# Performance work log

Hardware: AMD Instinct MI355X
Metric: run time of the kernel (lower is better)

Reference implementation:

```python
import jax, jax.numpy as jnp
import numpy as np

N_NODES = 50000


def _pointnet_layer(h, pos, src, dst, wA, bA, wB, bB):
    # message: MLP(concat(h_j, pos_j - pos_i)) per edge, then max-aggregate at dst
    m = jnp.concatenate([h[src], pos[src] - pos[dst]], axis=-1)  # [E, in+3]
    m = jax.nn.relu(m @ wA + bA) @ wB + bB                       # [E, out]
    agg = jax.ops.segment_max(m, dst, num_segments=N_NODES)     # [N, out]
    # PyG max-aggregation returns 0 for nodes with no incoming edges
    return jnp.where(jnp.isfinite(agg), agg, 0.0)


def setup_inputs() -> dict:
    key = jax.random.key(0)
    ks = jax.random.split(key, 16)
    num_points, num_features, E = 256, 256, 800000
    s = 0.05
    inp = {
        "x": jax.random.normal(ks[0], (N_NODES, num_points), dtype=jnp.float32),
        "pos": jax.random.normal(ks[1], (N_NODES, 3), dtype=jnp.float32),
        "edge_index": jax.random.randint(ks[2], (2, E), 0, N_NODES, dtype=jnp.int64),
        # conv1 mlp: (num_points+3 -> F -> F)
        "w1a": jax.random.normal(ks[3], (num_points + 3, num_features), dtype=jnp.float32) * s,
        "b1a": jnp.zeros((num_features,), dtype=jnp.float32),
        "w1b": jax.random.normal(ks[4], (num_features, num_features), dtype=jnp.float32) * s,
        "b1b": jnp.zeros((num_features,), dtype=jnp.float32),
        # conv2 mlp: (F+3 -> F -> F)
        "w2a": jax.random.normal(ks[5], (num_features + 3, num_features), dtype=jnp.float32) * s,
        "b2a": jnp.zeros((num_features,), dtype=jnp.float32),
        "w2b": jax.random.normal(ks[6], (num_features, num_features), dtype=jnp.float32) * s,
        "b2b": jnp.zeros((num_features,), dtype=jnp.float32),
        # decoder: F -> 256 -> num_points
        "wd1": jax.random.normal(ks[7], (num_features, 256), dtype=jnp.float32) * s,
        "bd1": jnp.zeros((256,), dtype=jnp.float32),
        "wd2": jax.random.normal(ks[8], (256, num_points), dtype=jnp.float32) * s,
        "bd2": jnp.zeros((num_points,), dtype=jnp.float32),
    }
    return inp


def reference(x, pos, edge_index, w1a, b1a, w1b, b1b, w2a, b2a, w2b, b2b, wd1, bd1, wd2, bd2):
    src, dst = edge_index[0], edge_index[1]  # message flows j(src) -> i(dst)
    h = jax.nn.relu(_pointnet_layer(x, pos, src, dst, w1a, b1a, w1b, b1b))
    h = jax.nn.relu(_pointnet_layer(h, pos, src, dst, w2a, b2a, w2b, b2b))
    decoded = jax.nn.relu(h @ wd1 + bd1) @ wd2 + bd2  # [N, num_points]
    return decoded
```

## Files before the change

kernel.cpp:

```cpp
#include <hip/hip_runtime.h>
#include <stdint.h>


using bf16x8 = __attribute__((ext_vector_type(8))) short;
using f32x4  = __attribute__((ext_vector_type(4))) float;

#define AB_STRIDE 40
#define ABUF      2560
#define ZSTRIDE   68

#define BARRIER_NOVM() asm volatile("s_waitcnt lgkmcnt(0)\n\ts_barrier" ::: "memory")

__device__ __forceinline__ float b2f(uint32_t v16) {
    return __uint_as_float(v16 << 16);
}
__device__ __forceinline__ float b2f_hi(uint32_t w) {
    return __uint_as_float(w & 0xffff0000u);
}
__device__ __forceinline__ uint16_t f2b(float f) {
    uint32_t u = __float_as_uint(f);
    u += 0x7fffu + ((u >> 16) & 1u);
    return (uint16_t)(u >> 16);
}
#if __has_builtin(__builtin_amdgcn_cvt_pk_bf16_f32)
__device__ __forceinline__ uint32_t pack2bf(float lo, float hi) {
    auto r = __builtin_amdgcn_cvt_pk_bf16_f32(lo, hi);
    uint32_t u; __builtin_memcpy(&u, &r, 4); return u;
}
#else
__device__ __forceinline__ uint32_t pack2bf(float lo, float hi) {
    return (uint32_t)f2b(lo) | ((uint32_t)f2b(hi) << 16);
}
#endif
__device__ __forceinline__ uint32_t encf(float f) {
    uint32_t u = __float_as_uint(f);
    return (u & 0x80000000u) ? ~u : (u | 0x80000000u);
}
__device__ __forceinline__ float decf(uint32_t k) {
    uint32_t u = (k & 0x80000000u) ? (k & 0x7fffffffu) : ~k;
    return __uint_as_float(u);
}

__global__ void detect_fmt(const uint32_t* __restrict__ x,
                           const uint32_t* __restrict__ ei,
                           uint32_t* __restrict__ flags) {
    if (threadIdx.x == 0 && blockIdx.x == 0) {
        int plaus = 0;
        for (int i = 0; i < 64; i++) {
            uint32_t v = x[i];
            uint32_t e = (v >> 23) & 0xffu;
            if (v == 0u || (e >= 96u && e <= 150u)) plaus++;
        }
        flags[0] = (plaus >= 48) ? 1u : 0u;
        int zeros = 0;
        for (int i = 0; i < 16; i++)
            if (ei[2 * i + 1] == 0u) zeros++;
        flags[1] = (zeros == 16) ? 1u : 0u;
    }
}

__global__ __launch_bounds__(256) void convert_big(
        const void* __restrict__ src, uint16_t* __restrict__ dst, int n,
        const uint32_t* __restrict__ flags) {
    bool isf32 = flags[0] != 0u;
    int i = (blockIdx.x * 256 + threadIdx.x) * 4;
    if (i + 3 < n) {
        if (isf32) {
            float4 v = ((const float4*)src)[i >> 2];
            uint2 o = {pack2bf(v.x, v.y), pack2bf(v.z, v.w)};
            ((uint2*)dst)[i >> 2] = o;
        } else {
            ((uint2*)dst)[i >> 2] = ((const uint2*)src)[i >> 2];
        }
    } else {
        for (int j = i; j < n; j++)
            dst[j] = isf32 ? f2b(((const float*)src)[j]) : ((const uint16_t*)src)[j];
    }
}

struct ConvArgs {
    const void* src[13];
    uint32_t dstOff[13];
    uint32_t n[13];
};

__global__ __launch_bounds__(256) void convert_small(
        ConvArgs a, uint16_t* __restrict__ dstBase, const uint32_t* __restrict__ flags) {
    bool isf32 = flags[0] != 0u;
    int t = blockIdx.y;
    int i = blockIdx.x * 256 + threadIdx.x;
    if (i >= (int)a.n[t]) return;
    uint16_t* d = dstBase + a.dstOff[t];
    d[i] = isf32 ? f2b(((const float*)a.src[t])[i]) : ((const uint16_t*)a.src[t])[i];
}

__global__ __launch_bounds__(256) void zero_i32(int* p, int n) {
    int i = blockIdx.x * 256 + threadIdx.x;
    if (i < n) p[i] = 0;
}

__global__ __launch_bounds__(256) void hist_dst(
        const int* __restrict__ ei_raw, int E, int* __restrict__ hist,
        const uint32_t* __restrict__ flags) {
    bool i64 = flags[1] != 0u;
    int e = blockIdx.x * 256 + threadIdx.x;
    if (e < E) {
        int d = i64 ? ei_raw[2 * (E + e)] : ei_raw[E + e];
        atomicAdd(&hist[d], 1);
    }
}

__global__ __launch_bounds__(1024) void scan_partial(
        const int* __restrict__ hist, int* __restrict__ cursor,
        int* __restrict__ part, int N) {
    __shared__ int wsum[16];
    int tid = threadIdx.x, lane = tid & 63, wid = tid >> 6;
    int base = blockIdx.x * 1024;
    int v = (base + tid < N) ? hist[base + tid] : 0;
    int x = v;
#pragma unroll
    for (int s = 1; s < 64; s <<= 1) {
        int t = __shfl_up(x, s, 64);
        if (lane >= s) x += t;
    }
    if (lane == 63) wsum[wid] = x;
    __syncthreads();
    if (wid == 0 && lane < 16) {
        int w = wsum[lane];
#pragma unroll
        for (int s = 1; s < 16; s <<= 1) {
            int t = __shfl_up(w, s, 64);
            if (lane >= s) w += t;
        }
        wsum[lane] = w;
    }
    __syncthreads();
    int wbase = (wid > 0) ? wsum[wid - 1] : 0;
    if (base + tid < N) cursor[base + tid] = x - v + wbase;
    if (tid == 0) part[blockIdx.x] = wsum[15];
}

__global__ __launch_bounds__(1024) void scan_carry(
        const int* __restrict__ part, int* __restrict__ carry, int B) {
    __shared__ int wsum[16];
    int tid = threadIdx.x, lane = tid & 63, wid = tid >> 6;
    int v = (tid < B) ? part[tid] : 0;
    int x = v;
#pragma unroll
    for (int s = 1; s < 64; s <<= 1) {
        int t = __shfl_up(x, s, 64);
        if (lane >= s) x += t;
    }
    if (lane == 63) wsum[wid] = x;
    __syncthreads();
    if (wid == 0 && lane < 16) {
        int w = wsum[lane];
#pragma unroll
        for (int s = 1; s < 16; s <<= 1) {
            int t = __shfl_up(w, s, 64);
            if (lane >= s) w += t;
        }
        wsum[lane] = w;
    }
    __syncthreads();
    int wbase = (wid > 0) ? wsum[wid - 1] : 0;
    if (tid < B) carry[tid] = x - v + wbase;
}

__global__ __launch_bounds__(1024) void scan_add(
        int* __restrict__ cursor, const int* __restrict__ carry, int N) {
    int i = blockIdx.x * 1024 + threadIdx.x;
    if (i < N) cursor[i] += carry[blockIdx.x];
}

__global__ __launch_bounds__(256) void scatter_edges(
        const int* __restrict__ ei_raw, int E, int* __restrict__ cursor,
        int* __restrict__ esrc, int* __restrict__ edst,
        const uint32_t* __restrict__ flags) {
    bool i64 = flags[1] != 0u;
    int e = blockIdx.x * 256 + threadIdx.x;
    if (e < E) {
        int s = i64 ? ei_raw[2 * e] : ei_raw[e];
        int d = i64 ? ei_raw[2 * (E + e)] : ei_raw[E + e];
        int p = atomicAdd(&cursor[d], 1);
        esrc[p] = s;
        edst[p] = d;
    }
}

__global__ __launch_bounds__(256) void transpose_w(
        const uint16_t* s0, const uint16_t* s1, const uint16_t* s2,
        const uint16_t* s3, const uint16_t* s4, const uint16_t* s5,
        uint16_t* dst) {
    const uint16_t* srcs[6] = {s0, s1, s2, s3, s4, s5};
    const uint16_t* src = srcs[blockIdx.y];
    uint16_t* d = dst + (size_t)blockIdx.y * 65536;
    int k = blockIdx.x;
    int n = threadIdx.x;
    d[(k >> 5) * 8192 + n * 32 + (k & 31)] = src[k * 256 + n];
}

__global__ __launch_bounds__(256) void pos_proj(
        const uint16_t* pos, const uint16_t* wpos, uint16_t* Q, int N) {
    int t = threadIdx.x;
    int r = t >> 5, c8 = (t & 31) * 8;
    int i = blockIdx.x * 8 + r;
    if (i >= N) return;
    uint4 wv0 = *(const uint4*)(wpos + c8);
    uint4 wv1 = *(const uint4*)(wpos + 256 + c8);
    uint4 wv2 = *(const uint4*)(wpos + 512 + c8);
    float p0 = b2f(pos[i * 3 + 0]);
    float p1 = b2f(pos[i * 3 + 1]);
    float p2 = b2f(pos[i * 3 + 2]);
    uint32_t w0[4] = {wv0.x, wv0.y, wv0.z, wv0.w};
    uint32_t w1[4] = {wv1.x, wv1.y, wv1.z, wv1.w};
    uint32_t w2[4] = {wv2.x, wv2.y, wv2.z, wv2.w};
    uint32_t o[4];
#pragma unroll
    for (int j = 0; j < 4; j++) {
        float lo = p0 * b2f(w0[j] & 0xffffu) + p1 * b2f(w1[j] & 0xffffu) + p2 * b2f(w2[j] & 0xffffu);
        float hi = p0 * b2f_hi(w0[j]) + p1 * b2f_hi(w1[j]) + p2 * b2f_hi(w2[j]);
        o[j] = pack2bf(lo, hi);
    }
    uint4 ov = {o[0], o[1], o[2], o[3]};
    *(uint4*)(Q + (size_t)i * 256 + c8) = ov;
}

__global__ __launch_bounds__(256) void init_agg(uint32_t* agg, int n4) {
    int i = blockIdx.x * 256 + threadIdx.x;
    if (i < n4) {
        uint4 v = {0x80000000u, 0x80000000u, 0x80000000u, 0x80000000u};
        ((uint4*)agg)[i] = v;
    }
}

template <int REINIT>
__global__ __launch_bounds__(256) void finalize_init(
        uint32_t* __restrict__ agg, uint16_t* __restrict__ h, int n4) {
    int i = blockIdx.x * 256 + threadIdx.x;
    if (i < n4) {
        uint4 a = ((uint4*)agg)[i];
        uint2 o = {pack2bf(decf(a.x), decf(a.y)), pack2bf(decf(a.z), decf(a.w))};
        ((uint2*)h)[i] = o;
        if (REINIT) {
            uint4 z = {0x80000000u, 0x80000000u, 0x80000000u, 0x80000000u};
            ((uint4*)agg)[i] = z;
        }
    }
}

template <int MODE>
__global__ __launch_bounds__(256) void gemm_node(
        const uint16_t* __restrict__ A, const uint16_t* __restrict__ BT,
        const uint16_t* __restrict__ bias, const uint16_t* __restrict__ Qadd,
        void* __restrict__ out, int M, const uint32_t* __restrict__ flags) {
    __shared__ __align__(16) uint16_t Al[2 * 64 * AB_STRIDE];
    int tid = threadIdx.x;
    int tileM = blockIdx.x;
    int wave = tid >> 6, lane = tid & 63, lrow = lane & 15, quad = lane >> 4;
    int row = tid >> 2, kq = (tid & 3) * 8;
    f32x4 acc[4][4] = {};

    int rg = tileM * 64 + row;
    bool rok = rg < M;
    const uint16_t* abase = A + (size_t)rg * 256 + kq;
    const uint16_t* bfrag = BT + (wave * 64 + lrow) * 32 + quad * 8;
    uint16_t* awr = Al + row * AB_STRIDE + kq;
    const uint16_t* ard = Al + lrow * AB_STRIDE + quad * 8;

    uint4 a0 = {0, 0, 0, 0};
    if (rok) a0 = *(const uint4*)abase;

#pragma unroll
    for (int kc = 0; kc < 256; kc += 32) {
        int buf = (kc >> 5) & 1;
        *(uint4*)(awr + buf * ABUF) = a0;
        const uint16_t* bp = bfrag + (kc >> 5) * 8192;
        bf16x8 bfv[4];
#pragma unroll
        for (int c = 0; c < 4; c++) bfv[c] = *(const bf16x8*)(bp + c * 512);
        if (kc < 224 && rok) a0 = *(const uint4*)(abase + kc + 32);
        BARRIER_NOVM();
        const uint16_t* ar = ard + buf * ABUF;
        bf16x8 af[4];
#pragma unroll
        for (int r = 0; r < 4; r++) af[r] = *(const bf16x8*)(ar + r * 16 * AB_STRIDE);
#pragma unroll
        for (int r = 0; r < 4; r++)
#pragma unroll
            for (int c = 0; c < 4; c++)
                acc[r][c] = __builtin_amdgcn_mfma_f32_16x16x32_bf16(af[r], bfv[c], acc[r][c], 0, 0, 0);
    }

    bool of32 = false;
    if (MODE == 2) of32 = flags[0] != 0u;

#pragma unroll
    for (int c = 0; c < 4; c++) {
        int col = wave * 64 + c * 16 + lrow;
        float bv = b2f(bias[col]);
#pragma unroll
        for (int r = 0; r < 4; r++) {
#pragma unroll
            for (int i = 0; i < 4; i++) {
                int rw = tileM * 64 + r * 16 + quad * 4 + i;
                if (rw >= M) continue;
                float v = acc[r][c][i] + bv;
                if (MODE == 0) {
                    v += b2f(Qadd[(size_t)rw * 256 + col]);
                    ((uint16_t*)out)[(size_t)rw * 256 + col] = f2b(v);
                } else if (MODE == 1) {
                    v = fmaxf(v, 0.f);
                    ((uint16_t*)out)[(size_t)rw * 256 + col] = f2b(v);
                } else {
                    if (of32) ((float*)out)[(size_t)rw * 256 + col] = v;
                    else      ((uint16_t*)out)[(size_t)rw * 256 + col] = f2b(v);
                }
            }
        }
    }
}

__global__ __launch_bounds__(256, 3) void edge_gemm_agg(
        const uint16_t* __restrict__ Gs16, const uint16_t* __restrict__ Qb,
        const uint16_t* __restrict__ BT, const uint16_t* __restrict__ bias,
        const int* __restrict__ esrc, const int* __restrict__ edst, int E,
        uint32_t* __restrict__ agg) {
    __shared__ __align__(16) uint16_t SM[256 * ZSTRIDE];
    uint16_t* Al = SM;
    uint16_t* Zl = SM;
    __shared__ int sdst[64];
    __shared__ uint64_t smask;
    int tid = threadIdx.x;
    int ebase = blockIdx.x * 64;
    int evalid = (E - ebase < 64) ? (E - ebase) : 64;
    if (tid < 64) sdst[tid] = (tid < evalid) ? edst[ebase + tid] : 0;

    int wave = tid >> 6, lane = tid & 63, lrow = lane & 15, quad = lane >> 4;
    int row = tid >> 2, kq = (tid & 3) * 8;
    int er = (row < evalid) ? row : (evalid - 1);
    int s = esrc[ebase + er];
    int d = edst[ebase + er];
    const uint16_t* gbase = Gs16 + (size_t)s * 256 + kq;
    const uint16_t* qbase = Qb   + (size_t)d * 256 + kq;
    const uint16_t* bfrag = BT + (wave * 64 + lrow) * 32 + quad * 8;
    uint16_t* awr = Al + row * AB_STRIDE + kq;
    const uint16_t* ard = Al + lrow * AB_STRIDE + quad * 8;

    f32x4 acc[4][4] = {};
    uint4 g = *(const uint4*)gbase;
    uint4 q = *(const uint4*)qbase;

#pragma unroll
    for (int kc = 0; kc < 256; kc += 32) {
        int buf = (kc >> 5) & 1;
        uint32_t gw[4] = {g.x, g.y, g.z, g.w};
        uint32_t qw[4] = {q.x, q.y, q.z, q.w};
        uint32_t mw[4];
#pragma unroll
        for (int j = 0; j < 4; j++) {
            float lo = fmaxf(b2f(gw[j] & 0xffffu) - b2f(qw[j] & 0xffffu), 0.f);
            float hi = fmaxf(b2f_hi(gw[j]) - b2f_hi(qw[j]), 0.f);
            mw[j] = pack2bf(lo, hi);
        }
        uint4 wv = {mw[0], mw[1], mw[2], mw[3]};
        *(uint4*)(awr + buf * ABUF) = wv;
        const uint16_t* bp = bfrag + (kc >> 5) * 8192;
        bf16x8 bfv[4];
#pragma unroll
        for (int c = 0; c < 4; c++) bfv[c] = *(const bf16x8*)(bp + c * 512);
        if (kc < 224) {
            g = *(const uint4*)(gbase + kc + 32);
            q = *(const uint4*)(qbase + kc + 32);
        }
        BARRIER_NOVM();
        const uint16_t* ar = ard + buf * ABUF;
        bf16x8 af[4];
#pragma unroll
        for (int r = 0; r < 4; r++) af[r] = *(const bf16x8*)(ar + r * 16 * AB_STRIDE);
#pragma unroll
        for (int r = 0; r < 4; r++)
#pragma unroll
            for (int c = 0; c < 4; c++)
                acc[r][c] = __builtin_amdgcn_mfma_f32_16x16x32_bf16(af[r], bfv[c], acc[r][c], 0, 0, 0);
    }
    __syncthreads();

    float bv[4];
#pragma unroll
    for (int c = 0; c < 4; c++) bv[c] = b2f(bias[wave * 64 + c * 16 + lrow]);
#pragma unroll
    for (int c = 0; c < 4; c++) {
        int col = wave * 64 + c * 16 + lrow;
#pragma unroll
        for (int r = 0; r < 4; r++) {
            uint2 z4 = {pack2bf(acc[r][c][0] + bv[c], acc[r][c][1] + bv[c]),
                        pack2bf(acc[r][c][2] + bv[c], acc[r][c][3] + bv[c])};
            *(uint2*)&Zl[col * ZSTRIDE + r * 16 + quad * 4] = z4;
        }
    }
    if (wave == 0) {
        int d0 = sdst[lane];
        int dp = (lane > 0) ? sdst[lane - 1] : -1;
        uint64_t m = __ballot(d0 != dp);
        if (lane == 0) smask = m;
    }
    __syncthreads();

    uint64_t mask = smask;
    int col = tid;
    const uint16_t* zc = &Zl[col * ZSTRIDE];
    float run = 0.f;
#pragma unroll 4
    for (int gi = 0; gi < 16; gi++) {
        int rbase = gi * 4;
        if (rbase >= evalid) break;
        uint2 z4 = *(const uint2*)&zc[rbase];
        float vv[4] = {b2f(z4.x & 0xffffu), b2f_hi(z4.x),
                       b2f(z4.y & 0xffffu), b2f_hi(z4.y)};
#pragma unroll
        for (int i = 0; i < 4; i++) {
            int r = rbase + i;
            if (r >= evalid) break;
            if (r == 0) {
                run = vv[0];
            } else if ((mask >> r) & 1ull) {
                int dp = sdst[r - 1];
                atomicMax(agg + (size_t)dp * 256 + col, encf(run));
                run = vv[i];
            } else {
                run = fmaxf(run, vv[i]);
            }
        }
    }
    if (evalid > 0)
        atomicMax(agg + (size_t)sdst[evalid - 1] * 256 + col, encf(run));
}

extern "C" void kernel_launch(void* const* d_in, const int* in_sizes, int n_in,
                              void* d_out, int out_size, void* d_ws, size_t ws_size,
                              hipStream_t stream) {
    const void* x_raw   = d_in[0];
    const void* pos_raw = d_in[1];
    const int*  ei_raw  = (const int*)d_in[2];

    int N = in_sizes[0] / 256;
    int E = in_sizes[2] / 2;

    char* ws = (char*)d_ws;
    size_t off = 0;
    auto alloc = [&](size_t bytes) { void* p = ws + off; off += (bytes + 255) & ~(size_t)255; return p; };

    uint32_t* flags = (uint32_t*)alloc(256);
    uint16_t* WT    = (uint16_t*)alloc(6 * 65536 * sizeof(uint16_t));
    const uint32_t POS_OFF = 0;
    const uint32_t W1A_OFF = POS_OFF + (uint32_t)(N * 3);
    const uint32_t W2A_OFF = W1A_OFF + 66304;
    const uint32_t W1B_OFF = W2A_OFF + 66304;
    const uint32_t W2B_OFF = W1B_OFF + 65536;
    const uint32_t WD1_OFF = W2B_OFF + 65536;
    const uint32_t WD2_OFF = WD1_OFF + 65536;
    const uint32_t B1A_OFF = WD2_OFF + 65536;
    const uint32_t B1B_OFF = B1A_OFF + 256;
    const uint32_t B2A_OFF = B1B_OFF + 256;
    const uint32_t B2B_OFF = B2A_OFF + 256;
    const uint32_t BD1_OFF = B2B_OFF + 256;
    const uint32_t BD2_OFF = BD1_OFF + 256;
    const uint32_t ARENA_ELEMS = BD2_OFF + 256;
    uint16_t* arena = (uint16_t*)alloc((size_t)ARENA_ELEMS * 2);
    int*      hist  = (int*)alloc((size_t)N * 4);
    int*      curs  = (int*)alloc((size_t)N * 4);
    int*      part  = (int*)alloc(1024 * 4);
    int*      carry = (int*)alloc(1024 * 4);
    int*      esrc  = (int*)alloc((size_t)E * 4);
    int*      edst  = (int*)alloc((size_t)E * 4);
    uint16_t* Qb    = (uint16_t*)alloc((size_t)N * 256 * 2);
    uint16_t* Gs    = (uint16_t*)alloc((size_t)N * 256 * 2);
    uint32_t* agg   = (uint32_t*)alloc((size_t)N * 256 * 4);
    uint16_t* xb    = (uint16_t*)alloc((size_t)N * 256 * 2);
    uint16_t* h     = xb;
    uint16_t* d1    = Gs;

    uint16_t* posb = arena + POS_OFF;
    uint16_t* w1a = arena + W1A_OFF, * w2a = arena + W2A_OFF;
    uint16_t* w1b = arena + W1B_OFF, * w2b = arena + W2B_OFF;
    uint16_t* wd1 = arena + WD1_OFF, * wd2 = arena + WD2_OFF;
    uint16_t* b1a = arena + B1A_OFF, * b1b = arena + B1B_OFF;
    uint16_t* b2a = arena + B2A_OFF, * b2b = arena + B2B_OFF;
    uint16_t* bd1 = arena + BD1_OFF, * bd2 = arena + BD2_OFF;

    int n4      = N * 64;
    int nbElem  = (n4 + 255) / 256;
    int nbNode  = (N + 63) / 64;
    int nbEdge  = (E + 63) / 64;
    int nbE256  = (E + 255) / 256;
    int nbPos   = (N + 7) / 8;
    int nbScan  = (N + 1023) / 1024;

    detect_fmt<<<1, 64, 0, stream>>>((const uint32_t*)x_raw, (const uint32_t*)ei_raw, flags);
    convert_big<<<(N * 256 / 4 + 255) / 256, 256, 0, stream>>>(x_raw, xb, N * 256, flags);

    ConvArgs ca;
    ca.src[0] = pos_raw;  ca.dstOff[0] = POS_OFF; ca.n[0] = (uint32_t)(N * 3);
    ca.src[1] = d_in[3];  ca.dstOff[1] = W1A_OFF; ca.n[1] = 66304;
    ca.src[2] = d_in[7];  ca.dstOff[2] = W2A_OFF; ca.n[2] = 66304;
    ca.src[3] = d_in[5];  ca.dstOff[3] = W1B_OFF; ca.n[3] = 65536;
    ca.src[4] = d_in[9];  ca.dstOff[4] = W2B_OFF; ca.n[4] = 65536;
    ca.src[5] = d_in[11]; ca.dstOff[5] = WD1_OFF; ca.n[5] = 65536;
    ca.src[6] = d_in[13]; ca.dstOff[6] = WD2_OFF; ca.n[6] = 65536;
    ca.src[7] = d_in[4];  ca.dstOff[7] = B1A_OFF; ca.n[7] = 256;
    ca.src[8] = d_in[6];  ca.dstOff[8] = B1B_OFF; ca.n[8] = 256;
    ca.src[9] = d_in[8];  ca.dstOff[9] = B2A_OFF; ca.n[9] = 256;
    ca.src[10] = d_in[10]; ca.dstOff[10] = B2B_OFF; ca.n[10] = 256;
    ca.src[11] = d_in[12]; ca.dstOff[11] = BD1_OFF; ca.n[11] = 256;
    ca.src[12] = d_in[14]; ca.dstOff[12] = BD2_OFF; ca.n[12] = 256;
    {
        uint32_t maxn = (uint32_t)(N * 3);
        dim3 g((maxn + 255) / 256, 13);
        convert_small<<<g, 256, 0, stream>>>(ca, arena, flags);
    }

    zero_i32<<<(N + 255) / 256, 256, 0, stream>>>(hist, N);
    hist_dst<<<nbE256, 256, 0, stream>>>(ei_raw, E, hist, flags);
    scan_partial<<<nbScan, 1024, 0, stream>>>(hist, curs, part, N);
    scan_carry<<<1, 1024, 0, stream>>>(part, carry, nbScan);
    scan_add<<<nbScan, 1024, 0, stream>>>(curs, carry, N);
    scatter_edges<<<nbE256, 256, 0, stream>>>(ei_raw, E, curs, esrc, edst, flags);

    transpose_w<<<dim3(256, 6), 256, 0, stream>>>(w1a, w1b, w2a, w2b, wd1, wd2, WT);

    pos_proj<<<nbPos, 256, 0, stream>>>(posb, w1a + 65536, Qb, N);
    gemm_node<0><<<nbNode, 256, 0, stream>>>(xb, WT + 0 * 65536, b1a, Qb, Gs, N, flags);
    init_agg<<<nbElem, 256, 0, stream>>>(agg, n4);
    edge_gemm_agg<<<nbEdge, 256, 0, stream>>>(Gs, Qb, WT + 1 * 65536, b1b, esrc, edst, E, agg);
    finalize_init<1><<<nbElem, 256, 0, stream>>>(agg, h, n4);

    pos_proj<<<nbPos, 256, 0, stream>>>(posb, w2a + 65536, Qb, N);
    gemm_node<0><<<nbNode, 256, 0, stream>>>(h, WT + 2 * 65536, b2a, Qb, Gs, N, flags);
    edge_gemm_agg<<<nbEdge, 256, 0, stream>>>(Gs, Qb, WT + 3 * 65536, b2b, esrc, edst, E, agg);
    finalize_init<0><<<nbElem, 256, 0, stream>>>(agg, h, n4);

    gemm_node<1><<<nbNode, 256, 0, stream>>>(h, WT + 4 * 65536, bd1, nullptr, d1, N, flags);
    gemm_node<2><<<nbNode, 256, 0, stream>>>(d1, WT + 5 * 65536, bd2, nullptr, d_out, N, flags);
}
```

Baseline: 766.4 us.

## Fuse input conversion, aggregation finalize and re-init into node GEMM prologues

Drops the standalone kernel that converts x to bf16 and the finalize/init_agg kernels. The node GEMMs now read raw f32 x or the encoded max-aggregation buffer directly and convert while staging tiles into LDS. The first aggregation buffer is reset to the sentinel inside the second layer's GEMM, and hist zeroing is merged with agg init. This removes several full passes over N×256 arrays and the intermediate bf16 h buffer. In exchange the GEMMs read 32-bit A data (twice the bytes), carry extra conversion ALU work, and get a launch_bounds occupancy hint; the in-place agg reset depends on each block rereading only its own rows.

```diff
diff --git a/kernel.cpp b/kernel.cpp
--- a/kernel.cpp
+++ b/kernel.cpp
@@ -59,25 +59,6 @@
     }
 }
 
-__global__ __launch_bounds__(256) void convert_big(
-        const void* __restrict__ src, uint16_t* __restrict__ dst, int n,
-        const uint32_t* __restrict__ flags) {
-    bool isf32 = flags[0] != 0u;
-    int i = (blockIdx.x * 256 + threadIdx.x) * 4;
-    if (i + 3 < n) {
-        if (isf32) {
-            float4 v = ((const float4*)src)[i >> 2];
-            uint2 o = {pack2bf(v.x, v.y), pack2bf(v.z, v.w)};
-            ((uint2*)dst)[i >> 2] = o;
-        } else {
-            ((uint2*)dst)[i >> 2] = ((const uint2*)src)[i >> 2];
-        }
-    } else {
-        for (int j = i; j < n; j++)
-            dst[j] = isf32 ? f2b(((const float*)src)[j]) : ((const uint16_t*)src)[j];
-    }
-}
-
 struct ConvArgs {
     const void* src[13];
     uint32_t dstOff[13];
@@ -94,9 +75,20 @@
     d[i] = isf32 ? f2b(((const float*)a.src[t])[i]) : ((const uint16_t*)a.src[t])[i];
 }
 
-__global__ __launch_bounds__(256) void zero_i32(int* p, int n) {
+__global__ __launch_bounds__(256) void init_hist_agg(
+        uint32_t* __restrict__ agg, int n4, int* __restrict__ hist, int N) {
     int i = blockIdx.x * 256 + threadIdx.x;
-    if (i < n) p[i] = 0;
+    if (i < n4) {
+        uint4 v = {0x80000000u, 0x80000000u, 0x80000000u, 0x80000000u};
+        ((uint4*)agg)[i] = v;
+    }
+    int i4 = i * 4;
+    if (i4 + 3 < N) {
+        uint4 z = {0, 0, 0, 0};
+        ((uint4*)hist)[i] = z;
+    } else if (i4 < N) {
+        for (int j = i4; j < N; j++) hist[j] = 0;
+    }
 }
 
 __global__ __launch_bounds__(256) void hist_dst(
@@ -226,34 +218,12 @@
     *(uint4*)(Q + (size_t)i * 256 + c8) = ov;
 }
 
-__global__ __launch_bounds__(256) void init_agg(uint32_t* agg, int n4) {
-    int i = blockIdx.x * 256 + threadIdx.x;
-    if (i < n4) {
-        uint4 v = {0x80000000u, 0x80000000u, 0x80000000u, 0x80000000u};
-        ((uint4*)agg)[i] = v;
-    }
-}
-
-template <int REINIT>
-__global__ __launch_bounds__(256) void finalize_init(
-        uint32_t* __restrict__ agg, uint16_t* __restrict__ h, int n4) {
-    int i = blockIdx.x * 256 + threadIdx.x;
-    if (i < n4) {
-        uint4 a = ((uint4*)agg)[i];
-        uint2 o = {pack2bf(decf(a.x), decf(a.y)), pack2bf(decf(a.z), decf(a.w))};
-        ((uint2*)h)[i] = o;
-        if (REINIT) {
-            uint4 z = {0x80000000u, 0x80000000u, 0x80000000u, 0x80000000u};
-            ((uint4*)agg)[i] = z;
-        }
-    }
-}
-
-template <int MODE>
-__global__ __launch_bounds__(256) void gemm_node(
-        const uint16_t* __restrict__ A, const uint16_t* __restrict__ BT,
+template <int AMODE, int OUTMODE, int REINIT>
+__global__ __launch_bounds__(256, 3) void gemm_node(
+        const void* __restrict__ Araw, const uint16_t* __restrict__ BT,
         const uint16_t* __restrict__ bias, const uint16_t* __restrict__ Qadd,
-        void* __restrict__ out, int M, const uint32_t* __restrict__ flags) {
+        void* __restrict__ out, int M, const uint32_t* __restrict__ flags,
+        uint32_t* __restrict__ aggwb) {
     __shared__ __align__(16) uint16_t Al[2 * 64 * AB_STRIDE];
     int tid = threadIdx.x;
     int tileM = blockIdx.x;
@@ -263,23 +233,61 @@
 
     int rg = tileM * 64 + row;
     bool rok = rg < M;
-    const uint16_t* abase = A + (size_t)rg * 256 + kq;
+    int rgc = rok ? rg : (M - 1);
+    bool isf32 = false;
+    if (AMODE == 2 || OUTMODE == 2) isf32 = flags[0] != 0u;
+
+    const uint16_t* a16 = (const uint16_t*)Araw + (size_t)rgc * 256 + kq;
+    const uint32_t* a32 = (const uint32_t*)Araw + (size_t)rgc * 256 + kq;
     const uint16_t* bfrag = BT + (wave * 64 + lrow) * 32 + quad * 8;
     uint16_t* awr = Al + row * AB_STRIDE + kq;
     const uint16_t* ard = Al + lrow * AB_STRIDE + quad * 8;
 
-    uint4 a0 = {0, 0, 0, 0};
-    if (rok) a0 = *(const uint4*)abase;
+    uint4 p0 = {0, 0, 0, 0}, p1 = {0, 0, 0, 0};
+    if (AMODE == 0) {
+        p0 = *(const uint4*)a16;
+    } else if (AMODE == 1) {
+        p0 = *(const uint4*)a32; p1 = *(const uint4*)(a32 + 4);
+    } else {
+        if (isf32) { p0 = *(const uint4*)a32; p1 = *(const uint4*)(a32 + 4); }
+        else       { p0 = *(const uint4*)a16; }
+    }
 
 #pragma unroll
     for (int kc = 0; kc < 256; kc += 32) {
         int buf = (kc >> 5) & 1;
-        *(uint4*)(awr + buf * ABUF) = a0;
+        uint4 wv;
+        if (AMODE == 0 || (AMODE == 2 && !isf32)) {
+            wv = p0;
+        } else if (AMODE == 1) {
+            uint32_t a[8] = {p0.x, p0.y, p0.z, p0.w, p1.x, p1.y, p1.z, p1.w};
+            wv.x = pack2bf(decf(a[0]), decf(a[1]));
+            wv.y = pack2bf(decf(a[2]), decf(a[3]));
+            wv.z = pack2bf(decf(a[4]), decf(a[5]));
+            wv.w = pack2bf(decf(a[6]), decf(a[7]));
+        } else {
+            wv.x = pack2bf(__uint_as_float(p0.x), __uint_as_float(p0.y));
+            wv.y = pack2bf(__uint_as_float(p0.z), __uint_as_float(p0.w));
+            wv.z = pack2bf(__uint_as_float(p1.x), __uint_as_float(p1.y));
+            wv.w = pack2bf(__uint_as_float(p1.z), __uint_as_float(p1.w));
+        }
+        *(uint4*)(awr + buf * ABUF) = wv;
         const uint16_t* bp = bfrag + (kc >> 5) * 8192;
         bf16x8 bfv[4];
 #pragma unroll
         for (int c = 0; c < 4; c++) bfv[c] = *(const bf16x8*)(bp + c * 512);
-        if (kc < 224 && rok) a0 = *(const uint4*)(abase + kc + 32);
+        if (kc < 224) {
+            if (AMODE == 0) {
+                p0 = *(const uint4*)(a16 + kc + 32);
+            } else if (AMODE == 1) {
+                p0 = *(const uint4*)(a32 + kc + 32);
+                p1 = *(const uint4*)(a32 + kc + 36);
+            } else {
+                if (isf32) { p0 = *(const uint4*)(a32 + kc + 32);
+                             p1 = *(const uint4*)(a32 + kc + 36); }
+                else       { p0 = *(const uint4*)(a16 + kc + 32); }
+            }
+        }
         BARRIER_NOVM();
         const uint16_t* ar = ard + buf * ABUF;
         bf16x8 af[4];
@@ -292,8 +300,15 @@
                 acc[r][c] = __builtin_amdgcn_mfma_f32_16x16x32_bf16(af[r], bfv[c], acc[r][c], 0, 0, 0);
     }
 
-    bool of32 = false;
-    if (MODE == 2) of32 = flags[0] != 0u;
+    if (AMODE == 1 && REINIT && rok) {
+        uint32_t* wb = aggwb + (size_t)rg * 256 + kq;
+        uint4 z = {0x80000000u, 0x80000000u, 0x80000000u, 0x80000000u};
+#pragma unroll
+        for (int kc = 0; kc < 256; kc += 32) {
+            *(uint4*)(wb + kc) = z;
+            *(uint4*)(wb + kc + 4) = z;
+        }
+    }
 
 #pragma unroll
     for (int c = 0; c < 4; c++) {
@@ -306,15 +321,15 @@
                 int rw = tileM * 64 + r * 16 + quad * 4 + i;
                 if (rw >= M) continue;
                 float v = acc[r][c][i] + bv;
-                if (MODE == 0) {
+                if (OUTMODE == 0) {
                     v += b2f(Qadd[(size_t)rw * 256 + col]);
                     ((uint16_t*)out)[(size_t)rw * 256 + col] = f2b(v);
-                } else if (MODE == 1) {
+                } else if (OUTMODE == 1) {
                     v = fmaxf(v, 0.f);
                     ((uint16_t*)out)[(size_t)rw * 256 + col] = f2b(v);
                 } else {
-                    if (of32) ((float*)out)[(size_t)rw * 256 + col] = v;
-                    else      ((uint16_t*)out)[(size_t)rw * 256 + col] = f2b(v);
+                    if (isf32) ((float*)out)[(size_t)rw * 256 + col] = v;
+                    else       ((uint16_t*)out)[(size_t)rw * 256 + col] = f2b(v);
                 }
             }
         }
@@ -477,8 +492,6 @@
     uint16_t* Qb    = (uint16_t*)alloc((size_t)N * 256 * 2);
     uint16_t* Gs    = (uint16_t*)alloc((size_t)N * 256 * 2);
     uint32_t* agg   = (uint32_t*)alloc((size_t)N * 256 * 4);
-    uint16_t* xb    = (uint16_t*)alloc((size_t)N * 256 * 2);
-    uint16_t* h     = xb;
     uint16_t* d1    = Gs;
 
     uint16_t* posb = arena + POS_OFF;
@@ -498,7 +511,6 @@
     int nbScan  = (N + 1023) / 1024;
 
     detect_fmt<<<1, 64, 0, stream>>>((const uint32_t*)x_raw, (const uint32_t*)ei_raw, flags);
-    convert_big<<<(N * 256 / 4 + 255) / 256, 256, 0, stream>>>(x_raw, xb, N * 256, flags);
 
     ConvArgs ca;
     ca.src[0] = pos_raw;  ca.dstOff[0] = POS_OFF; ca.n[0] = (uint32_t)(N * 3);
@@ -520,7 +532,7 @@
         convert_small<<<g, 256, 0, stream>>>(ca, arena, flags);
     }
 
-    zero_i32<<<(N + 255) / 256, 256, 0, stream>>>(hist, N);
+    init_hist_agg<<<nbElem, 256, 0, stream>>>(agg, n4, hist, N);
     hist_dst<<<nbE256, 256, 0, stream>>>(ei_raw, E, hist, flags);
     scan_partial<<<nbScan, 1024, 0, stream>>>(hist, curs, part, N);
     scan_carry<<<1, 1024, 0, stream>>>(part, carry, nbScan);
@@ -530,16 +542,17 @@
     transpose_w<<<dim3(256, 6), 256, 0, stream>>>(w1a, w1b, w2a, w2b, wd1, wd2, WT);
 
     pos_proj<<<nbPos, 256, 0, stream>>>(posb, w1a + 65536, Qb, N);
-    gemm_node<0><<<nbNode, 256, 0, stream>>>(xb, WT + 0 * 65536, b1a, Qb, Gs, N, flags);
-    init_agg<<<nbElem, 256, 0, stream>>>(agg, n4);
+    gemm_node<2, 0, 0><<<nbNode, 256, 0, stream>>>(
+        x_raw, WT + 0 * 65536, b1a, Qb, Gs, N, flags, nullptr);
     edge_gemm_agg<<<nbEdge, 256, 0, stream>>>(Gs, Qb, WT + 1 * 65536, b1b, esrc, edst, E, agg);
-    finalize_init<1><<<nbElem, 256, 0, stream>>>(agg, h, n4);
 
     pos_proj<<<nbPos, 256, 0, stream>>>(posb, w2a + 65536, Qb, N);
-    gemm_node<0><<<nbNode, 256, 0, stream>>>(h, WT + 2 * 65536, b2a, Qb, Gs, N, flags);
+    gemm_node<1, 0, 1><<<nbNode, 256, 0, stream>>>(
+        agg, WT + 2 * 65536, b2a, Qb, Gs, N, flags, agg);
     edge_gemm_agg<<<nbEdge, 256, 0, stream>>>(Gs, Qb, WT + 3 * 65536, b2b, esrc, edst, E, agg);
-    finalize_init<0><<<nbElem, 256, 0, stream>>>(agg, h, n4);
-
-    gemm_node<1><<<nbNode, 256, 0, stream>>>(h, WT + 4 * 65536, bd1, nullptr, d1, N, flags);
-    gemm_node<2><<<nbNode, 256, 0, stream>>>(d1, WT + 5 * 65536, bd2, nullptr, d_out, N, flags);
-}
+
+    gemm_node<1, 1, 0><<<nbNode, 256, 0, stream>>>(
+        agg, WT + 4 * 65536, bd1, nullptr, d1, N, flags, nullptr);
+    gemm_node<0, 2, 0><<<nbNode, 256, 0, stream>>>(
+        d1, WT + 5 * 65536, bd2, nullptr, d_out, N, flags, nullptr);
+}
```

Result: faster. 710.5 us (-7.3%).
